# Optimization experiments

Hardware: AMD Instinct MI355X
Metric: run time of the kernel (lower is better)

## Reference

```python
import math
import jax, jax.numpy as jnp
import numpy as np

B, T, C, H = 4, 1024, 1024, 16
HD = C // H
BLOCK = 1024


def setup_inputs() -> dict:
    key = jax.random.key(0)
    k0, k1, k2, k3 = jax.random.split(key, 4)
    x = jax.random.normal(k0, (B, T, C), dtype=jnp.float32)
    # torch Linear weight is (out, in); we store (in, out) and apply x @ W + b
    W_attn = jax.random.normal(k1, (C, 3 * C), dtype=jnp.float32) * 0.02
    b_attn = jnp.zeros((3 * C,), dtype=jnp.float32)
    W_proj = jax.random.normal(k2, (C, C), dtype=jnp.float32) * 0.02
    b_proj = jnp.zeros((C,), dtype=jnp.float32)
    # rel_pos_emb: (n_head, block_size, head_dim), std 0.02 (leading 1 dim dropped)
    rel_pos_emb = jax.random.normal(k3, (H, BLOCK, HD), dtype=jnp.float32) * 0.02
    return {"x": x, "W_attn": W_attn, "b_attn": b_attn,
            "W_proj": W_proj, "b_proj": b_proj, "rel_pos_emb": rel_pos_emb}


def reference(x, W_attn, b_attn, W_proj, b_proj, rel_pos_emb):
    Bx, Tx, Cx = x.shape
    qkv = x @ W_attn + b_attn                      # (B, T, 3C)
    q, k, v = jnp.split(qkv, 3, axis=2)
    q = q.reshape(Bx, Tx, H, HD).transpose(0, 2, 1, 3)   # (B, H, T, hd)
    k = k.reshape(Bx, Tx, H, HD).transpose(0, 2, 1, 3)
    v = v.reshape(Bx, Tx, H, HD).transpose(0, 2, 1, 3)

    att = jnp.einsum('bhid,bhjd->bhij', q, k)      # (B, H, T, T)

    # relative position score: pos[b,h,i,j] = sum_d E[h, clamp(i-j,0), d] * k[b,h,j,d]
    # compute P[b,h,r,j] = <E[h,r,:], k[b,h,j,:]> then gather r = clamp(i-j, 0)
    rng = jnp.arange(Tx)
    dist = jnp.clip(rng[:, None] - rng[None, :], 0, None)          # (T, T)
    P = jnp.einsum('hrd,bhjd->bhrj', rel_pos_emb[:, :Tx], k)       # (B, H, T, T)
    pos_score = jnp.take_along_axis(P, dist[None, None, :, :], axis=2)
    att = att + pos_score

    att = att * (1.0 / math.sqrt(HD))
    causal = jnp.tril(jnp.ones((Tx, Tx), dtype=bool))
    att = jnp.where(causal[None, None], att, -jnp.inf)
    att = jax.nn.softmax(att, axis=-1)
    # dropout p=0.0 -> identity
    y = jnp.einsum('bhij,bhjd->bhid', att, v)      # (B, H, T, hd)
    y = y.transpose(0, 2, 1, 3).reshape(Bx, Tx, Cx)
    return y @ W_proj + b_proj
```

## Files before the change

### kernel.cpp

```cpp
#include <hip/hip_runtime.h>


typedef __bf16 bf16x8 __attribute__((ext_vector_type(8)));
typedef float f32x4 __attribute__((ext_vector_type(4)));
typedef unsigned short ushort_t;

#define T_SEQ 1024
#define NHEAD 16
#define HDIM 64
#define PLANE 4194304

__device__ __forceinline__ float bf2f(ushort_t h) {
    unsigned int u = ((unsigned int)h) << 16;
    float f; __builtin_memcpy(&f, &u, 4); return f;
}
__device__ __forceinline__ ushort_t f2bf(float f) {
    __bf16 h = (__bf16)f;
    ushort_t u; __builtin_memcpy(&u, &h, 2); return u;
}

__global__ __launch_bounds__(256) void sentinel_kernel(float* out, int n, float val) {
    const int i = blockIdx.x * 256 + threadIdx.x;
    if (i < n) out[i] = val;
}

__global__ __launch_bounds__(256) void prep(
    const float* __restrict__ x, ushort_t* __restrict__ x16,
    const float* __restrict__ E, ushort_t* __restrict__ E16,
    const float* __restrict__ Wa, ushort_t* __restrict__ WaT,
    const float* __restrict__ Wp, ushort_t* __restrict__ WpT)
{
    __shared__ ushort_t t[64][65];
    const int bid = blockIdx.x;
    if (bid < 5120) {
        const float* src; ushort_t* dst; int base;
        if (bid < 4096) { src = x; dst = x16; base = bid * 1024; }
        else            { src = E; dst = E16; base = (bid - 4096) * 1024; }
        const int i = base + (int)threadIdx.x * 4;
        const float4 v = *reinterpret_cast<const float4*>(src + i);
        union { unsigned long long u; ushort_t s[4]; } o;
        o.s[0] = f2bf(v.x); o.s[1] = f2bf(v.y); o.s[2] = f2bf(v.z); o.s[3] = f2bf(v.w);
        *reinterpret_cast<unsigned long long*>(dst + i) = o.u;
        return;
    }
    const float* W; ushort_t* Wt; int Kdim, Ndim, n0, k0;
    if (bid < 5888) {
        const int r = bid - 5120;
        W = Wa; Wt = WaT; Kdim = 1024; Ndim = 3072;
        n0 = (r % 48) * 64; k0 = (r / 48) * 64;
    } else {
        const int r = bid - 5888;
        W = Wp; Wt = WpT; Kdim = 1024; Ndim = 1024;
        n0 = (r % 16) * 64; k0 = (r / 16) * 64;
    }
    const int cx = threadIdx.x & 63, ry = threadIdx.x >> 6;
#pragma unroll
    for (int i = 0; i < 16; i++) {
        const int r = ry + i * 4;
        t[r][cx] = f2bf(W[(size_t)(k0 + r) * Ndim + n0 + cx]);
    }
    __syncthreads();
#pragma unroll
    for (int i = 0; i < 16; i++) {
        const int r = ry + i * 4;
        Wt[(size_t)(n0 + r) * Kdim + k0 + cx] = t[cx][r];
    }
}

__global__ __launch_bounds__(256) void transpose_v(
    const ushort_t* __restrict__ v, ushort_t* __restrict__ vT)
{
    __shared__ ushort_t t[64][65];
    const int bh = blockIdx.y;
    const int t0 = blockIdx.x * 64;
    const int cx = threadIdx.x & 63, ry = threadIdx.x >> 6;
    const ushort_t* src = v + (size_t)bh * 65536;
    ushort_t* dst = vT + (size_t)bh * 65536;
#pragma unroll
    for (int i = 0; i < 16; i++) {
        const int r = ry + i * 4;
        t[r][cx] = src[(size_t)(t0 + r) * HDIM + cx];
    }
    __syncthreads();
#pragma unroll
    for (int i = 0; i < 16; i++) {
        const int d = ry + i * 4;
        dst[(size_t)d * T_SEQ + t0 + cx] = t[cx][d];
    }
}

template <int MODE, int BN>
__global__ __launch_bounds__(256) void gemm128(
    const ushort_t* __restrict__ A16, const ushort_t* __restrict__ Bt,
    const float* __restrict__ bias, void* __restrict__ out_,
    int Ndim, int Kdim)
{
    constexpr int NT = BN / 32;
    __shared__ __align__(16) ushort_t As[128 * 32];
    __shared__ __align__(16) ushort_t Bs[BN * 32];

    const int tid = threadIdx.x;
    const int w = tid >> 6;
    const int lane = tid & 63;
    const int l15 = lane & 15;
    const int quad = lane >> 4;
    const int m0 = blockIdx.y * 128, n0 = blockIdx.x * BN;
    const int wm = (w & 1) * 64, wn = (w >> 1) * (BN / 2);

    f32x4 acc[4][NT];
#pragma unroll
    for (int mt = 0; mt < 4; mt++)
#pragma unroll
        for (int nt = 0; nt < NT; nt++) acc[mt][nt] = (f32x4){0.f, 0.f, 0.f, 0.f};

    for (int kk = 0; kk < Kdim; kk += 32) {
        __syncthreads();
#pragma unroll
        for (int t = 0; t < 2; t++) {
            const int chunk = w * 128 + t * 64 + lane;
            const int row = chunk >> 2, kc = (chunk & 3) * 8;
            __builtin_amdgcn_global_load_lds(
                (const __attribute__((address_space(1))) void*)
                    (A16 + (size_t)(m0 + row) * Kdim + kk + kc),
                (__attribute__((address_space(3))) void*)
                    (As + (size_t)(w * 128 + t * 64) * 8), 16, 0, 0);
            if (BN == 128)
                __builtin_amdgcn_global_load_lds(
                    (const __attribute__((address_space(1))) void*)
                        (Bt + (size_t)(n0 + row) * Kdim + kk + kc),
                    (__attribute__((address_space(3))) void*)
                        (Bs + (size_t)(w * 128 + t * 64) * 8), 16, 0, 0);
        }
        if (BN == 64) {
            const int chunk = w * 64 + lane;
            const int row = chunk >> 2, kc = (chunk & 3) * 8;
            __builtin_amdgcn_global_load_lds(
                (const __attribute__((address_space(1))) void*)
                    (Bt + (size_t)(n0 + row) * Kdim + kk + kc),
                (__attribute__((address_space(3))) void*)
                    (Bs + (size_t)(w * 64) * 8), 16, 0, 0);
        }
        __syncthreads();

        bf16x8 af[4], bf[NT];
#pragma unroll
        for (int mt = 0; mt < 4; mt++)
            af[mt] = *reinterpret_cast<const bf16x8*>(&As[(wm + mt * 16 + l15) * 32 + quad * 8]);
#pragma unroll
        for (int nt = 0; nt < NT; nt++)
            bf[nt] = *reinterpret_cast<const bf16x8*>(&Bs[(wn + nt * 16 + l15) * 32 + quad * 8]);
#pragma unroll
        for (int mt = 0; mt < 4; mt++)
#pragma unroll
            for (int nt = 0; nt < NT; nt++)
                acc[mt][nt] = __builtin_amdgcn_mfma_f32_16x16x32_bf16(
                    af[mt], bf[nt], acc[mt][nt], 0, 0, 0);
    }

#pragma unroll
    for (int mt = 0; mt < 4; mt++)
#pragma unroll
        for (int nt = 0; nt < NT; nt++) {
            const int n = n0 + wn + nt * 16 + l15;
            const float bv = bias[n];
#pragma unroll
            for (int r = 0; r < 4; r++) {
                const int m = m0 + wm + mt * 16 + quad * 4 + r;
                const float val = acc[mt][nt][r] + bv;
                if (MODE == 0) {
                    ushort_t* ws = (ushort_t*)out_;
                    const int which = n >> 10;
                    const size_t pl = (which == 2) ? 3 : which;
                    const int cc = n & 1023;
                    const int h = cc >> 6, d = cc & 63;
                    const int bb = m >> 10, t = m & 1023;
                    ws[pl * PLANE + ((size_t)(bb * NHEAD + h) * T_SEQ + t) * HDIM + d] = f2bf(val);
                } else {
                    ((float*)out_)[(size_t)m * Ndim + n] = val;
                }
            }
        }
}

__global__ __launch_bounds__(256) void flash_attn(
    const ushort_t* __restrict__ qp, const ushort_t* __restrict__ kp,
    const ushort_t* __restrict__ vTp, const ushort_t* __restrict__ E16,
    ushort_t* __restrict__ y16)
{
    __shared__ __align__(16) ushort_t Ks[64 * 64];
    __shared__ __align__(16) ushort_t Vt[64 * 64];
    __shared__ __align__(16) ushort_t Es[128 * 64];
    __shared__ __align__(16) ushort_t Ps[64 * 64];

    const int bh = blockIdx.x;
    const int h = bh & (NHEAD - 1);
    const int b = bh >> 4;
    const int it = 15 - (int)blockIdx.y;
    const int tid = threadIdx.x;
    const int w = tid >> 6;
    const int lane = tid & 63;
    const int l15 = lane & 15;
    const int quad = lane >> 4;

    const size_t base = (size_t)bh * T_SEQ * HDIM;
    const ushort_t* Eh = E16 + (size_t)h * T_SEQ * HDIM;
    const ushort_t* vTb = vTp + (size_t)bh * 65536;
    const float c1 = 0.125f * 1.44269504f;

    const int rq = tid >> 2, cq = (tid & 3) * 16;
    const int re = tid >> 1, ce = (tid & 1) * 32;

    const int kswz = (l15 & 7) << 3;
    const int swr  = (rq & 7) << 3;
    const int swe  = (re & 7) << 3;
    const int jswz = quad << 4;

    bf16x8 ones;
#pragma unroll
    for (int i = 0; i < 8; i++) ones[i] = (__bf16)1.0f;

    const int i0 = it * 64;

    bf16x8 qf[2];
    {
        const ushort_t* qrow = qp + base + (size_t)(i0 + w * 16 + l15) * HDIM;
        qf[0] = *reinterpret_cast<const bf16x8*>(qrow + quad * 8);
        qf[1] = *reinterpret_cast<const bf16x8*>(qrow + 32 + quad * 8);
    }

    f32x4 o[4], o5;
#pragma unroll
    for (int dt = 0; dt < 4; dt++) o[dt] = (f32x4){0.f, 0.f, 0.f, 0.f};
    o5 = (f32x4){0.f, 0.f, 0.f, 0.f};
    float mrow[4];
#pragma unroll
    for (int r = 0; r < 4; r++) mrow[r] = -3e38f;

    for (int j0 = 0; j0 <= i0; j0 += 64) {
        const int d0 = i0 - j0;
        __syncthreads();
        {
            const ushort_t* ksrc = kp + base + (size_t)(j0 + rq) * HDIM + cq;
            *reinterpret_cast<uint4*>(&Ks[rq * 64 + (cq ^ swr)]) = *reinterpret_cast<const uint4*>(ksrc);
            *reinterpret_cast<uint4*>(&Ks[rq * 64 + ((cq + 8) ^ swr)]) = *reinterpret_cast<const uint4*>(ksrc + 8);
            const ushort_t* vsrc = vTb + (size_t)rq * T_SEQ + j0 + cq;
            *reinterpret_cast<uint4*>(&Vt[rq * 64 + (cq ^ swr)]) = *reinterpret_cast<const uint4*>(vsrc);
            *reinterpret_cast<uint4*>(&Vt[rq * 64 + ((cq + 8) ^ swr)]) = *reinterpret_cast<const uint4*>(vsrc + 8);
        }
        {
            int g = d0 - 64 + re;
            g = g < 0 ? 0 : (g > 1023 ? 1023 : g);
            const ushort_t* esrc = Eh + (size_t)g * HDIM + ce;
#pragma unroll
            for (int q16 = 0; q16 < 4; q16++)
                *reinterpret_cast<uint4*>(&Es[re * 64 + ((ce + q16 * 8) ^ swe)]) =
                    *reinterpret_cast<const uint4*>(esrc + q16 * 8);
        }
        __syncthreads();

        f32x4 s[4], pb[2][4];
#pragma unroll
        for (int nt = 0; nt < 4; nt++) {
            s[nt] = (f32x4){0.f, 0.f, 0.f, 0.f};
            pb[0][nt] = (f32x4){0.f, 0.f, 0.f, 0.f};
            pb[1][nt] = (f32x4){0.f, 0.f, 0.f, 0.f};
        }
        __builtin_amdgcn_s_setprio(1);
#pragma unroll
        for (int ks = 0; ks < 2; ks++) {
            const int ko = ks * 32 + quad * 8;
            const bf16x8 ae0 = *reinterpret_cast<const bf16x8*>(&Es[(w * 32 + l15) * 64 + (ko ^ kswz)]);
            const bf16x8 ae1 = *reinterpret_cast<const bf16x8*>(&Es[(w * 32 + 16 + l15) * 64 + (ko ^ kswz)]);
#pragma unroll
            for (int nt = 0; nt < 4; nt++) {
                const bf16x8 bk = *reinterpret_cast<const bf16x8*>(&Ks[(nt * 16 + l15) * 64 + (ko ^ kswz)]);
                s[nt] = __builtin_amdgcn_mfma_f32_16x16x32_bf16(qf[ks], bk, s[nt], 0, 0, 0);
                pb[0][nt] = __builtin_amdgcn_mfma_f32_16x16x32_bf16(ae0, bk, pb[0][nt], 0, 0, 0);
                pb[1][nt] = __builtin_amdgcn_mfma_f32_16x16x32_bf16(ae1, bk, pb[1][nt], 0, 0, 0);
            }
        }
        __builtin_amdgcn_s_setprio(0);
#pragma unroll
        for (int mf = 0; mf < 2; mf++)
#pragma unroll
            for (int nt = 0; nt < 4; nt++) {
                const int jl = nt * 16 + l15;
#pragma unroll
                for (int r = 0; r < 4; r++) {
                    const int br = w * 32 + mf * 16 + quad * 4 + r;
                    const int il_t = br - 64 + jl;
                    if ((unsigned)il_t < 64u)
                        Ps[il_t * 64 + (jl ^ (((il_t >> 2) & 3) << 4))] = f2bf(pb[mf][nt][r]);
                }
            }
        __syncthreads();

        float pv[4][4], mnew[4];
#pragma unroll
        for (int r = 0; r < 4; r++) mnew[r] = mrow[r];
        const int il0 = w * 16 + quad * 4;
        if (j0 < i0) {
#pragma unroll
            for (int nt = 0; nt < 4; nt++) {
                const int jl = nt * 16 + l15;
#pragma unroll
                for (int r = 0; r < 4; r++) {
                    const float sv = (s[nt][r] + bf2f(Ps[(il0 + r) * 64 + (jl ^ jswz)])) * c1;
                    pv[nt][r] = sv;
                    mnew[r] = fmaxf(mnew[r], sv);
                }
            }
        } else {
#pragma unroll
            for (int nt = 0; nt < 4; nt++) {
                const int jl = nt * 16 + l15;
#pragma unroll
                for (int r = 0; r < 4; r++) {
                    const int il = il0 + r;
                    float sv = (s[nt][r] + bf2f(Ps[il * 64 + (jl ^ jswz)])) * c1;
                    if (jl > il) sv = -3e38f;
                    pv[nt][r] = sv;
                    mnew[r] = fmaxf(mnew[r], sv);
                }
            }
        }
#pragma unroll
        for (int r = 0; r < 4; r++)
#pragma unroll
            for (int off = 1; off < 16; off <<= 1)
                mnew[r] = fmaxf(mnew[r], __shfl_xor(mnew[r], off, 64));
        float alpha[4];
#pragma unroll
        for (int r = 0; r < 4; r++) {
            alpha[r] = exp2f(mrow[r] - mnew[r]);
            mrow[r] = mnew[r];
        }
#pragma unroll
        for (int nt = 0; nt < 4; nt++)
#pragma unroll
            for (int r = 0; r < 4; r++)
                pv[nt][r] = exp2f(pv[nt][r] - mnew[r]);
#pragma unroll
        for (int dt = 0; dt < 4; dt++)
#pragma unroll
            for (int r = 0; r < 4; r++) o[dt][r] *= alpha[r];
#pragma unroll
        for (int r = 0; r < 4; r++) o5[r] *= alpha[r];
#pragma unroll
        for (int nt = 0; nt < 4; nt++)
#pragma unroll
            for (int r = 0; r < 4; r++) {
                const int rr = w * 16 + quad * 4 + r;
                Ks[rr * 64 + ((nt * 16 + l15) ^ ((rr & 7) << 3))] = f2bf(pv[nt][r]);
            }

        __builtin_amdgcn_s_setprio(1);
#pragma unroll
        for (int ks = 0; ks < 2; ks++) {
            const int ko = ks * 32 + quad * 8;
            const bf16x8 ap = *reinterpret_cast<const bf16x8*>(&Ks[(w * 16 + l15) * 64 + (ko ^ kswz)]);
#pragma unroll
            for (int dt = 0; dt < 4; dt++) {
                const bf16x8 bv = *reinterpret_cast<const bf16x8*>(&Vt[(dt * 16 + l15) * 64 + (ko ^ kswz)]);
                o[dt] = __builtin_amdgcn_mfma_f32_16x16x32_bf16(ap, bv, o[dt], 0, 0, 0);
            }
            o5 = __builtin_amdgcn_mfma_f32_16x16x32_bf16(ap, ones, o5, 0, 0, 0);
        }
        __builtin_amdgcn_s_setprio(0);
    }

    float inv[4];
#pragma unroll
    for (int r = 0; r < 4; r++) inv[r] = 1.0f / o5[r];
#pragma unroll
    for (int dt = 0; dt < 4; dt++)
#pragma unroll
        for (int r = 0; r < 4; r++) {
            const int il = w * 16 + quad * 4 + r;
            const int d = dt * 16 + l15;
            y16[((size_t)(b * T_SEQ + i0 + il)) * 1024 + h * 64 + d] = f2bf(o[dt][r] * inv[r]);
        }
}

extern "C" void kernel_launch(void* const* d_in, const int* in_sizes, int n_in,
                              void* d_out, int out_size, void* d_ws, size_t ws_size,
                              hipStream_t stream) {
    float* out = (float*)d_out;

    const void* x = nullptr; const void* Wa = nullptr; const void* ba = nullptr;
    const void* Wp = nullptr; const void* bp = nullptr; const void* E = nullptr;
    int anomaly = 0;
    if (n_in != 6) {
        anomaly = 2;
    } else {
        int c1M = 0;
        for (int i = 0; i < 6; i++) {
            const int s = in_sizes[i];
            if      (s == 4194304) x  = d_in[i];
            else if (s == 3145728) Wa = d_in[i];
            else if (s == 3072)    ba = d_in[i];
            else if (s == 1024)    bp = d_in[i];
            else if (s == 1048576) { if (c1M == 0) Wp = d_in[i]; else E = d_in[i]; c1M++; }
            else anomaly = 1;
        }
        if (!x || !Wa || !ba || !Wp || !bp || !E || c1M != 2) anomaly = 1;
    }
    if (!anomaly && out_size != 4194304) anomaly = 3;
    if (!anomaly && ws_size < (size_t)52428800) anomaly = 4;
    if (anomaly) {
        sentinel_kernel<<<(out_size + 255) / 256, 256, 0, stream>>>(out, out_size, 1000.0f * anomaly);
        return;
    }

    ushort_t* ws   = (ushort_t*)d_ws;
    ushort_t* qp   = ws;
    ushort_t* kp   = ws + (size_t)PLANE;
    ushort_t* vTp  = ws + (size_t)2 * PLANE;
    ushort_t* vtmp = ws + (size_t)3 * PLANE;
    ushort_t* y16  = vtmp;
    ushort_t* x16  = ws + (size_t)4 * PLANE;
    ushort_t* WaT  = ws + (size_t)5 * PLANE;
    ushort_t* WpT  = WaT + (size_t)3145728;
    ushort_t* E16  = WpT + (size_t)1048576;

    prep<<<6144, 256, 0, stream>>>((const float*)x, x16, (const float*)E, E16,
                                   (const float*)Wa, WaT, (const float*)Wp, WpT);

    gemm128<0, 128><<<dim3(24, 32), 256, 0, stream>>>(x16, WaT, (const float*)ba, (void*)ws, 3072, 1024);

    transpose_v<<<dim3(16, 64), 256, 0, stream>>>(vtmp, vTp);

    flash_attn<<<dim3(64, 16), 256, 0, stream>>>(qp, kp, vTp, E16, y16);

    gemm128<1, 64><<<dim3(16, 32), 256, 0, stream>>>(y16, WpT, (const float*)bp, (void*)out, 1024, 1024);
}
```

Measured before the change: 213.0 us.

## Pair causal query tiles per block and double-buffer K/V/E with register prefetch

Each attention block now processes two query tiles (it and 15-it), so every block runs exactly 17 key-tile steps and the causal triangle is balanced across a grid of half the size. The K, V^T and E tiles are double-buffered in shared memory: global loads for the next step are issued into registers before the current step's MFMAs and written to the alternate buffer afterwards, leaving one barrier per step. The probability tile now goes to its own Ps buffer instead of reusing Ks. This costs about twice the LDS and more registers, which can lower occupancy, and halves the number of blocks.

```diff
diff --git a/kernel.cpp b/kernel.cpp
--- a/kernel.cpp
+++ b/kernel.cpp
@@ -187,15 +187,18 @@
     const ushort_t* __restrict__ vTp, const ushort_t* __restrict__ E16,
     ushort_t* __restrict__ y16)
 {
-    __shared__ __align__(16) ushort_t Ks[64 * 64];
-    __shared__ __align__(16) ushort_t Vt[64 * 64];
-    __shared__ __align__(16) ushort_t Es[128 * 64];
+    __shared__ __align__(16) ushort_t Ks[2][64 * 64];
+    __shared__ __align__(16) ushort_t Vt[2][64 * 64];
+    __shared__ __align__(16) ushort_t Es[2][128 * 64];
     __shared__ __align__(16) ushort_t Ps[64 * 64];
 
     const int bh = blockIdx.x;
     const int h = bh & (NHEAD - 1);
     const int b = bh >> 4;
-    const int it = 15 - (int)blockIdx.y;
+    const int by = blockIdx.y;
+    const int ita = 15 - by, itb = by;
+    const int n1 = ita + 1;
+
     const int tid = threadIdx.x;
     const int w = tid >> 6;
     const int lane = tid & 63;
@@ -219,44 +222,80 @@
 #pragma unroll
     for (int i = 0; i < 8; i++) ones[i] = (__bf16)1.0f;
 
-    const int i0 = it * 64;
-
+    auto seq = [&](int u, int& i0, int& j0) {
+        if (u < n1) { i0 = ita * 64; j0 = u * 64; }
+        else        { i0 = itb * 64; j0 = (u - n1) * 64; }
+    };
+
+    uint4 pf[8];
+    auto issue_loads = [&](int u) {
+        int i0u, j0u; seq(u, i0u, j0u);
+        const int d0u = i0u - j0u;
+        const ushort_t* ksrc = kp + base + (size_t)(j0u + rq) * HDIM + cq;
+        pf[0] = *reinterpret_cast<const uint4*>(ksrc);
+        pf[1] = *reinterpret_cast<const uint4*>(ksrc + 8);
+        const ushort_t* vsrc = vTb + (size_t)rq * T_SEQ + j0u + cq;
+        pf[2] = *reinterpret_cast<const uint4*>(vsrc);
+        pf[3] = *reinterpret_cast<const uint4*>(vsrc + 8);
+        int g = d0u - 64 + re;
+        g = g < 0 ? 0 : (g > 1023 ? 1023 : g);
+        const ushort_t* esrc = Eh + (size_t)g * HDIM + ce;
+#pragma unroll
+        for (int q16 = 0; q16 < 4; q16++)
+            pf[4 + q16] = *reinterpret_cast<const uint4*>(esrc + q16 * 8);
+    };
+    auto write_stage = [&](int bb) {
+        *reinterpret_cast<uint4*>(&Ks[bb][rq * 64 + (cq ^ swr)]) = pf[0];
+        *reinterpret_cast<uint4*>(&Ks[bb][rq * 64 + ((cq + 8) ^ swr)]) = pf[1];
+        *reinterpret_cast<uint4*>(&Vt[bb][rq * 64 + (cq ^ swr)]) = pf[2];
+        *reinterpret_cast<uint4*>(&Vt[bb][rq * 64 + ((cq + 8) ^ swr)]) = pf[3];
+#pragma unroll
+        for (int q16 = 0; q16 < 4; q16++)
+            *reinterpret_cast<uint4*>(&Es[bb][re * 64 + ((ce + q16 * 8) ^ swe)]) = pf[4 + q16];
+    };
+
+    f32x4 o[4], o5;
+    float mrow[4];
+    float inv[4];
     bf16x8 qf[2];
-    {
+
+    auto reset_state = [&](int i0) {
+#pragma unroll
+        for (int dt = 0; dt < 4; dt++) o[dt] = (f32x4){0.f, 0.f, 0.f, 0.f};
+        o5 = (f32x4){0.f, 0.f, 0.f, 0.f};
+#pragma unroll
+        for (int r = 0; r < 4; r++) mrow[r] = -3e38f;
         const ushort_t* qrow = qp + base + (size_t)(i0 + w * 16 + l15) * HDIM;
         qf[0] = *reinterpret_cast<const bf16x8*>(qrow + quad * 8);
         qf[1] = *reinterpret_cast<const bf16x8*>(qrow + 32 + quad * 8);
-    }
-
-    f32x4 o[4], o5;
-#pragma unroll
-    for (int dt = 0; dt < 4; dt++) o[dt] = (f32x4){0.f, 0.f, 0.f, 0.f};
-    o5 = (f32x4){0.f, 0.f, 0.f, 0.f};
-    float mrow[4];
-#pragma unroll
-    for (int r = 0; r < 4; r++) mrow[r] = -3e38f;
-
-    for (int j0 = 0; j0 <= i0; j0 += 64) {
-        const int d0 = i0 - j0;
-        __syncthreads();
-        {
-            const ushort_t* ksrc = kp + base + (size_t)(j0 + rq) * HDIM + cq;
-            *reinterpret_cast<uint4*>(&Ks[rq * 64 + (cq ^ swr)]) = *reinterpret_cast<const uint4*>(ksrc);
-            *reinterpret_cast<uint4*>(&Ks[rq * 64 + ((cq + 8) ^ swr)]) = *reinterpret_cast<const uint4*>(ksrc + 8);
-            const ushort_t* vsrc = vTb + (size_t)rq * T_SEQ + j0 + cq;
-            *reinterpret_cast<uint4*>(&Vt[rq * 64 + (cq ^ swr)]) = *reinterpret_cast<const uint4*>(vsrc);
-            *reinterpret_cast<uint4*>(&Vt[rq * 64 + ((cq + 8) ^ swr)]) = *reinterpret_cast<const uint4*>(vsrc + 8);
-        }
-        {
-            int g = d0 - 64 + re;
-            g = g < 0 ? 0 : (g > 1023 ? 1023 : g);
-            const ushort_t* esrc = Eh + (size_t)g * HDIM + ce;
-#pragma unroll
-            for (int q16 = 0; q16 < 4; q16++)
-                *reinterpret_cast<uint4*>(&Es[re * 64 + ((ce + q16 * 8) ^ swe)]) =
-                    *reinterpret_cast<const uint4*>(esrc + q16 * 8);
-        }
-        __syncthreads();
+    };
+    auto epilogue = [&](int i0) {
+#pragma unroll
+        for (int r = 0; r < 4; r++) inv[r] = 1.0f / o5[r];
+#pragma unroll
+        for (int dt = 0; dt < 4; dt++)
+#pragma unroll
+            for (int r = 0; r < 4; r++) {
+                const int il = w * 16 + quad * 4 + r;
+                const int d = dt * 16 + l15;
+                y16[((size_t)(b * T_SEQ + i0 + il)) * 1024 + h * 64 + d] =
+                    f2bf(o[dt][r] * inv[r]);
+            }
+    };
+
+    issue_loads(0);
+    write_stage(0);
+    reset_state(ita * 64);
+    __syncthreads();
+
+    for (int u = 0; u < 17; ++u) {
+        const int bb = u & 1;
+        int i0, j0; seq(u, i0, j0);
+        if (u == n1) {
+            epilogue(ita * 64);
+            reset_state(itb * 64);
+        }
+        if (u + 1 < 17) issue_loads(u + 1);
 
         f32x4 s[4], pb[2][4];
 #pragma unroll
@@ -269,11 +308,11 @@
 #pragma unroll
         for (int ks = 0; ks < 2; ks++) {
             const int ko = ks * 32 + quad * 8;
-            const bf16x8 ae0 = *reinterpret_cast<const bf16x8*>(&Es[(w * 32 + l15) * 64 + (ko ^ kswz)]);
-            const bf16x8 ae1 = *reinterpret_cast<const bf16x8*>(&Es[(w * 32 + 16 + l15) * 64 + (ko ^ kswz)]);
+            const bf16x8 ae0 = *reinterpret_cast<const bf16x8*>(&Es[bb][(w * 32 + l15) * 64 + (ko ^ kswz)]);
+            const bf16x8 ae1 = *reinterpret_cast<const bf16x8*>(&Es[bb][(w * 32 + 16 + l15) * 64 + (ko ^ kswz)]);
 #pragma unroll
             for (int nt = 0; nt < 4; nt++) {
-                const bf16x8 bk = *reinterpret_cast<const bf16x8*>(&Ks[(nt * 16 + l15) * 64 + (ko ^ kswz)]);
+                const bf16x8 bk = *reinterpret_cast<const bf16x8*>(&Ks[bb][(nt * 16 + l15) * 64 + (ko ^ kswz)]);
                 s[nt] = __builtin_amdgcn_mfma_f32_16x16x32_bf16(qf[ks], bk, s[nt], 0, 0, 0);
                 pb[0][nt] = __builtin_amdgcn_mfma_f32_16x16x32_bf16(ae0, bk, pb[0][nt], 0, 0, 0);
                 pb[1][nt] = __builtin_amdgcn_mfma_f32_16x16x32_bf16(ae1, bk, pb[1][nt], 0, 0, 0);
@@ -351,35 +390,29 @@
 #pragma unroll
             for (int r = 0; r < 4; r++) {
                 const int rr = w * 16 + quad * 4 + r;
-                Ks[rr * 64 + ((nt * 16 + l15) ^ ((rr & 7) << 3))] = f2bf(pv[nt][r]);
-            }
+                Ps[rr * 64 + ((nt * 16 + l15) ^ ((rr & 7) << 3))] = f2bf(pv[nt][r]);
+            }
+
+        if (u + 1 < 17) write_stage(bb ^ 1);
 
         __builtin_amdgcn_s_setprio(1);
 #pragma unroll
         for (int ks = 0; ks < 2; ks++) {
             const int ko = ks * 32 + quad * 8;
-            const bf16x8 ap = *reinterpret_cast<const bf16x8*>(&Ks[(w * 16 + l15) * 64 + (ko ^ kswz)]);
+            const bf16x8 ap = *reinterpret_cast<const bf16x8*>(&Ps[(w * 16 + l15) * 64 + (ko ^ kswz)]);
 #pragma unroll
             for (int dt = 0; dt < 4; dt++) {
-                const bf16x8 bv = *reinterpret_cast<const bf16x8*>(&Vt[(dt * 16 + l15) * 64 + (ko ^ kswz)]);
+                const bf16x8 bv = *reinterpret_cast<const bf16x8*>(&Vt[bb][(dt * 16 + l15) * 64 + (ko ^ kswz)]);
                 o[dt] = __builtin_amdgcn_mfma_f32_16x16x32_bf16(ap, bv, o[dt], 0, 0, 0);
             }
             o5 = __builtin_amdgcn_mfma_f32_16x16x32_bf16(ap, ones, o5, 0, 0, 0);
         }
         __builtin_amdgcn_s_setprio(0);
-    }
-
-    float inv[4];
-#pragma unroll
-    for (int r = 0; r < 4; r++) inv[r] = 1.0f / o5[r];
-#pragma unroll
-    for (int dt = 0; dt < 4; dt++)
-#pragma unroll
-        for (int r = 0; r < 4; r++) {
-            const int il = w * 16 + quad * 4 + r;
-            const int d = dt * 16 + l15;
-            y16[((size_t)(b * T_SEQ + i0 + il)) * 1024 + h * 64 + d] = f2bf(o[dt][r] * inv[r]);
-        }
+
+        __syncthreads();
+    }
+
+    epilogue(itb * 64);
 }
 
 extern "C" void kernel_launch(void* const* d_in, const int* in_sizes, int n_in,
@@ -430,7 +463,7 @@
 
     transpose_v<<<dim3(16, 64), 256, 0, stream>>>(vtmp, vTp);
 
-    flash_attn<<<dim3(64, 16), 256, 0, stream>>>(qp, kp, vTp, E16, y16);
+    flash_attn<<<dim3(64, 8), 256, 0, stream>>>(qp, kp, vTp, E16, y16);
 
     gemm128<1, 64><<<dim3(16, 32), 256, 0, stream>>>(y16, WpT, (const float*)bp, (void*)out, 1024, 1024);
 }
```

Result: slower. 259.3 us (+21.7%).
